# Performance work log

Measured on AMD Instinct MI355X. Metric: run time of the kernel, lower is better.

The kernel has to match this reference:

```python
import jax, jax.numpy as jnp
import numpy as np

B, N, C = 4, 4096, 768
H = 8
HD = C // H  # head_dim = 96
SCALE = HD ** -0.5
EPS = 1e-12  # torch F.normalize eps


def setup_inputs() -> dict:
    key = jax.random.key(0)
    ks = jax.random.split(key, 6)
    s = C ** -0.5
    return {
        "context_x": jax.random.normal(ks[0], (B, N, C), dtype=jnp.float32),
        "depth_x": jax.random.normal(ks[1], (B, N, C), dtype=jnp.float32),
        "Wq": jax.random.normal(ks[2], (C, C), dtype=jnp.float32) * s,
        "Wkv": jax.random.normal(ks[3], (C, 2 * C), dtype=jnp.float32) * s,
        "Wproj": jax.random.normal(ks[4], (C, C), dtype=jnp.float32) * s,
        "bproj": jax.random.normal(ks[5], (C,), dtype=jnp.float32) * 0.01,
    }


def _l2norm(x):
    # matches torch.nn.functional.normalize(x, dim=-1)
    n = jnp.sqrt(jnp.sum(x * x, axis=-1, keepdims=True))
    return x / jnp.maximum(n, EPS)


def reference(context_x, depth_x, Wq, Wkv, Wproj, bproj):
    b, n, c = context_x.shape
    # projections
    q = (context_x @ Wq).reshape(b, n, H, HD).transpose(0, 2, 3, 1)  # [B,H,hd,N]
    kv = (depth_x @ Wkv).reshape(b, n, 2, H, HD)
    k = kv[:, :, 0].transpose(0, 2, 3, 1)  # [B,H,hd,N]
    v = kv[:, :, 1].transpose(0, 2, 3, 1)  # [B,H,hd,N]
    # cosine-normalize over the token axis (last dim after transpose)
    q = _l2norm(q)
    k = _l2norm(k)
    # channel-attention (cross-covariance): attn is [B,H,hd,hd]
    attn = jnp.einsum("bhdn,bhen->bhde", q, k) * SCALE
    attn = jax.nn.softmax(attn, axis=-1)
    x = jnp.einsum("bhde,bhen->bhdn", attn, v)  # [B,H,hd,N]
    x = x.transpose(0, 3, 1, 2).reshape(b, n, c)  # [B,N,C]
    return x @ Wproj + bproj
```

## Files before the change

kernel.cpp:

```cpp
#include <hip/hip_runtime.h>


using bf16x8 = __attribute__((ext_vector_type(8))) short;
using f32x4  = __attribute__((ext_vector_type(4))) float;

#define SCALE_ 0.10206207261596575f

__device__ __forceinline__ unsigned short f2bf(float f) {
    unsigned int u = __builtin_bit_cast(unsigned int, f);
    u += 0x7FFFu + ((u >> 16) & 1u);
    return (unsigned short)(u >> 16);
}
__device__ __forceinline__ float bf2f(unsigned short h) {
    unsigned int u = ((unsigned int)h) << 16;
    return __builtin_bit_cast(float, u);
}

__device__ __forceinline__ void glds16(const unsigned short* g, unsigned short* l) {
    __builtin_amdgcn_global_load_lds(
        (const __attribute__((address_space(1))) void*)g,
        (__attribute__((address_space(3))) void*)l, 16, 0, 0);
}

__device__ __forceinline__ float ssq8(bf16x8 v) {
    uint4 u = __builtin_bit_cast(uint4, v);
    unsigned a[4] = {u.x, u.y, u.z, u.w};
    float s = 0.f;
    #pragma unroll
    for (int i = 0; i < 4; i++) {
        float lo = __builtin_bit_cast(float, a[i] << 16);
        float hi = __builtin_bit_cast(float, a[i] & 0xFFFF0000u);
        s += lo * lo + hi * hi;
    }
    return s;
}

__global__ void f32_to_bf16_k(const float* __restrict__ in,
                              unsigned short* __restrict__ out)
{
    size_t idx = ((size_t)blockIdx.x * 256 + threadIdx.x) * 8;
    float4 v0 = *(const float4*)&in[idx];
    float4 v1 = *(const float4*)&in[idx + 4];
    unsigned short h[8];
    h[0] = f2bf(v0.x); h[1] = f2bf(v0.y); h[2] = f2bf(v0.z); h[3] = f2bf(v0.w);
    h[4] = f2bf(v1.x); h[5] = f2bf(v1.y); h[6] = f2bf(v1.z); h[7] = f2bf(v1.w);
    *(bf16x8*)&out[idx] = *(bf16x8*)h;
}

__global__ void transpose_to_bf16(const float* __restrict__ W,
                                  unsigned short* __restrict__ Wt,
                                  int K, int N)
{
    __shared__ float tile[32][33];
    int n0 = blockIdx.x * 32, k0 = blockIdx.y * 32;
    int tx = threadIdx.x, ty = threadIdx.y;
    #pragma unroll
    for (int i = 0; i < 32; i += 8)
        tile[ty + i][tx] = W[(size_t)(k0 + ty + i) * N + n0 + tx];
    __syncthreads();
    #pragma unroll
    for (int i = 0; i < 32; i += 8)
        Wt[(size_t)(n0 + ty + i) * K + k0 + tx] = f2bf(tile[tx][ty + i]);
}


#define BAR __builtin_amdgcn_s_barrier()
#define VM(n) asm volatile("s_waitcnt vmcnt(" #n ")" ::: "memory")

#define ST_A(buf, tt, h) do { \
    _Pragma("unroll") \
    for (int c_ = 0; c_ < 2; c_++) \
        glds16(gA + (size_t)(((h) * 8 + w) * 16) * K + (size_t)(tt) * 64 + c_ * 32, \
               &As[buf][(c_ * 16 + (h) * 8 + w) * 512]); \
} while (0)

#define ST_B(buf, tt, h) do { \
    _Pragma("unroll") \
    for (int c_ = 0; c_ < 2; c_++) \
        glds16(gB + (size_t)(((h) * 8 + w) * 16) * K + (size_t)(tt) * 64 + c_ * 32, \
               &Bs[buf][(c_ * 16 + (h) * 8 + w) * 512]); \
} while (0)

#define RD_A(buf, mh) do { \
    _Pragma("unroll") \
    for (int i_ = 0; i_ < 4; i_++) \
    _Pragma("unroll") \
    for (int kk_ = 0; kk_ < 2; kk_++) \
        a[i_][kk_] = *(const bf16x8*)&As[buf][(kk_ * 16 + wr * 8 + (mh) * 4 + i_) * 512 + lane * 8]; \
} while (0)

#define RD_B(buf, nh) do { \
    _Pragma("unroll") \
    for (int j_ = 0; j_ < 2; j_++) \
    _Pragma("unroll") \
    for (int kk_ = 0; kk_ < 2; kk_++) \
        b[nh][j_][kk_] = *(const bf16x8*)&Bs[buf][(kk_ * 16 + wc * 4 + (nh) * 2 + j_) * 512 + lane * 8]; \
} while (0)

#define MM(mh, nh) do { \
    __builtin_amdgcn_s_setprio(1); \
    _Pragma("unroll") \
    for (int i_ = 0; i_ < 4; i_++) \
    _Pragma("unroll") \
    for (int j_ = 0; j_ < 2; j_++) \
    _Pragma("unroll") \
    for (int kk_ = 0; kk_ < 2; kk_++) \
        acc[(mh) * 4 + i_][(nh) * 2 + j_] = __builtin_amdgcn_mfma_f32_16x16x32_bf16( \
            a[i_][kk_], b[nh][j_][kk_], acc[(mh) * 4 + i_][(nh) * 2 + j_], 0, 0, 0); \
    __builtin_amdgcn_s_setprio(0); \
} while (0)

#define KITER(t0v, LAST) do { \
     RD_A(0, 0); RD_B(0, 0); ST_B(1, (t0v) + 1, 0); \
             BAR; MM(0, 0); BAR; \
     RD_B(0, 1); ST_B(1, (t0v) + 1, 1); \
             BAR; MM(0, 1); VM(6); BAR; \
     RD_A(0, 1); ST_A(1, (t0v) + 1, 1); \
             BAR; MM(1, 0); BAR; \
     if (!(LAST)) ST_A(0, (t0v) + 2, 0); \
             BAR; MM(1, 1); if (LAST) { VM(2); } else { VM(4); } BAR; \
     RD_A(1, 0); RD_B(1, 0); if (!(LAST)) ST_B(0, (t0v) + 2, 0); \
             BAR; MM(0, 0); BAR; \
     RD_B(1, 1); if (!(LAST)) ST_B(0, (t0v) + 2, 1); \
             BAR; MM(0, 1); if (LAST) { VM(0); } else { VM(6); } BAR; \
     RD_A(1, 1); if (!(LAST)) ST_A(0, (t0v) + 2, 1); \
             BAR; MM(1, 0); BAR; \
     if (!(LAST)) { ST_A(1, (t0v) + 3, 0); } \
             BAR; MM(1, 1); if (!(LAST)) { VM(4); } BAR; \
} while (0)

template<int MODE>
__global__ __launch_bounds__(512, 2) void gemm_bt(
    const unsigned short* __restrict__ A, const unsigned short* __restrict__ Bt,
    const float* __restrict__ bias, void* __restrict__ out0, void* __restrict__ out1,
    int M, int N, int K)
{
    __shared__ unsigned short As[2][32 * 512];
    __shared__ unsigned short Bs[2][32 * 512];

    const int Nt = gridDim.x, Mt = gridDim.y;
    const int lin = blockIdx.y * Nt + blockIdx.x;
    const int xcd = lin & 7, li = lin >> 3;
    const int band = Mt >> 3;
    const int mt = xcd * band + (li % band);
    const int nt = li / band;
    const int bm = mt * 256, bn = nt * 256;

    const int t = threadIdx.x, lane = t & 63, w = t >> 6;
    const int wr = w >> 2, wc = w & 3;
    const int mf = lane & 15, quad = lane >> 4;
    const int srow = lane & 15, skc = (lane >> 4) * 8;

    const unsigned short* gA = A  + (size_t)(bm + srow) * K + skc;
    const unsigned short* gB = Bt + (size_t)(bn + srow) * K + skc;

    f32x4 acc[8][4] = {};
    bf16x8 a[4][2], b[2][2][2];

    const int NIT = K >> 7;

    ST_A(0, 0, 0); ST_A(0, 0, 1); ST_B(0, 0, 0); ST_B(0, 0, 1); ST_A(1, 1, 0);
    VM(2); BAR;

    for (int it = 0; it < NIT - 1; ++it) { KITER(2 * it, false); }
    KITER(2 * (NIT - 1), true);

    if constexpr (MODE == 2) {
        float* C = (float*)out0;
        #pragma unroll
        for (int i = 0; i < 8; i++) {
            int row0 = bm + wr * 128 + i * 16 + quad * 4;
            #pragma unroll
            for (int j = 0; j < 4; j++) {
                int col = bn + wc * 64 + j * 16 + mf;
                float bv = bias[col];
                #pragma unroll
                for (int r = 0; r < 4; r++)
                    C[(size_t)(row0 + r) * N + col] = acc[i][j][r] + bv;
            }
        }
    } else {
        unsigned short* Tr = (unsigned short*)out0;
        unsigned short* Vb = (unsigned short*)out1;
        const bool kpart = (MODE == 0) || (bn < 768);
        #pragma unroll
        for (int i = 0; i < 8; i++) {
            int row0 = bm + wr * 128 + i * 16 + quad * 4;
            int bb = row0 >> 12, n = row0 & 4095;
            #pragma unroll
            for (int j = 0; j < 4; j++) {
                int c = bn + wc * 64 + j * 16 + mf;
                if (kpart) {
                    int h = (c * 683) >> 16;
                    int d = c - h * 96;
                    size_t o = ((size_t)((bb * 8 + h) * 96 + d)) * 4096 + n;
                    ushort4 v4;
                    v4.x = f2bf(acc[i][j][0]); v4.y = f2bf(acc[i][j][1]);
                    v4.z = f2bf(acc[i][j][2]); v4.w = f2bf(acc[i][j][3]);
                    *(ushort4*)&Tr[o] = v4;
                } else {
                    int cv = c - 768;
                    #pragma unroll
                    for (int r = 0; r < 4; r++)
                        Vb[(size_t)(row0 + r) * 768 + cv] = f2bf(acc[i][j][r]);
                }
            }
        }
    }
}

#undef KITER
#undef MM
#undef RD_A
#undef RD_B
#undef ST_A
#undef ST_B
#undef VM
#undef BAR

__global__ __launch_bounds__(256) void s_gemm(
    const unsigned short* __restrict__ Qt, const unsigned short* __restrict__ Kt,
    float* __restrict__ Spart, float* __restrict__ ssq)
{
    __shared__ unsigned short Qs[2][12 * 512];
    __shared__ unsigned short Ks[2][12 * 512];
    const int s = blockIdx.x, bh = blockIdx.y;
    const int t = threadIdx.x, lane = t & 63, w = t >> 6;
    const int m0 = (w >> 1) * 48, n0w = (w & 1) * 48;
    const int mf = lane & 15, quad = lane >> 4;
    const int srow = lane & 15, skc = (lane >> 4) * 8;
    const int nwin = s * 512;

    const unsigned short* Qg = Qt + (size_t)bh * 96 * 4096;
    const unsigned short* Kg = Kt + (size_t)bh * 96 * 4096;

    f32x4 acc[3][3] = {};
    float sq[3] = {0.f, 0.f, 0.f}, sk[3] = {0.f, 0.f, 0.f};

    #pragma unroll
    for (int c = 0; c < 3; c++) {
        int bi = w * 3 + c, kc = bi / 6, g = bi % 6;
        size_t go = (size_t)(g * 16 + srow) * 4096 + nwin + kc * 32 + skc;
        glds16(Qg + go, &Qs[0][bi * 512]);
        glds16(Kg + go, &Ks[0][bi * 512]);
    }

    for (int it = 0; it < 8; it++) {
        const int cur = it & 1;
        __syncthreads();
        if (it + 1 < 8) {
            const int nxt = cur ^ 1;
            const int nn = nwin + (it + 1) * 64;
            #pragma unroll
            for (int c = 0; c < 3; c++) {
                int bi = w * 3 + c, kc = bi / 6, g = bi % 6;
                size_t go = (size_t)(g * 16 + srow) * 4096 + nn + kc * 32 + skc;
                glds16(Qg + go, &Qs[nxt][bi * 512]);
                glds16(Kg + go, &Ks[nxt][bi * 512]);
            }
        }
        #pragma unroll
        for (int kk = 0; kk < 2; kk++) {
            bf16x8 a[3], b[3];
            #pragma unroll
            for (int i = 0; i < 3; i++)
                a[i] = *(const bf16x8*)&Qs[cur][(kk * 6 + (w >> 1) * 3 + i) * 512 + lane * 8];
            #pragma unroll
            for (int j = 0; j < 3; j++)
                b[j] = *(const bf16x8*)&Ks[cur][(kk * 6 + (w & 1) * 3 + j) * 512 + lane * 8];
            if ((w & 1) == 0) {
                #pragma unroll
                for (int i = 0; i < 3; i++) sq[i] += ssq8(a[i]);
            }
            if ((w >> 1) == 0) {
                #pragma unroll
                for (int j = 0; j < 3; j++) sk[j] += ssq8(b[j]);
            }
            #pragma unroll
            for (int i = 0; i < 3; i++)
                #pragma unroll
                for (int j = 0; j < 3; j++)
                    acc[i][j] = __builtin_amdgcn_mfma_f32_16x16x32_bf16(a[i], b[j], acc[i][j], 0, 0, 0);
        }
    }

    if ((w & 1) == 0) {
        #pragma unroll
        for (int i = 0; i < 3; i++) {
            float v = sq[i];
            v += __shfl_xor(v, 16, 64);
            v += __shfl_xor(v, 32, 64);
            if (lane < 16) atomicAdd(&ssq[bh * 96 + m0 + i * 16 + lane], v);
        }
    }
    if ((w >> 1) == 0) {
        #pragma unroll
        for (int j = 0; j < 3; j++) {
            float v = sk[j];
            v += __shfl_xor(v, 16, 64);
            v += __shfl_xor(v, 32, 64);
            if (lane < 16) atomicAdd(&ssq[3072 + bh * 96 + n0w + j * 16 + lane], v);
        }
    }

    float* outp = Spart + (size_t)(bh * 8 + s) * 9216;
    #pragma unroll
    for (int i = 0; i < 3; i++)
        #pragma unroll
        for (int j = 0; j < 3; j++) {
            int e  = n0w + j * 16 + mf;
            int d0 = m0 + i * 16 + quad * 4;
            #pragma unroll
            for (int r = 0; r < 4; r++)
                outp[(d0 + r) * 96 + e] = acc[i][j][r];
        }
}

__global__ __launch_bounds__(256) void softmax_k(
    const float* __restrict__ Spart, const float* __restrict__ ssq,
    unsigned short* __restrict__ P)
{
    const int bh = blockIdx.y;
    const int d  = blockIdx.x * 4 + (threadIdx.x >> 6);
    const int lane = threadIdx.x & 63;

    const float sr = SCALE_ / fmaxf(sqrtf(ssq[bh * 96 + d]), 1e-12f);

    const float* Sp = Spart + (size_t)bh * 8 * 9216 + d * 96;
    float sa = 0.f, sb = 0.f;
    #pragma unroll
    for (int ch = 0; ch < 8; ch++) {
        sa += Sp[ch * 9216 + lane];
        if (lane < 32) sb += Sp[ch * 9216 + 64 + lane];
    }
    float ka = 1.0f / fmaxf(sqrtf(ssq[3072 + bh * 96 + lane]), 1e-12f);
    float va = sa * sr * ka;
    float vb = -1e30f;
    if (lane < 32) {
        float kb = 1.0f / fmaxf(sqrtf(ssq[3072 + bh * 96 + 64 + lane]), 1e-12f);
        vb = sb * sr * kb;
    }

    float m = fmaxf(va, vb);
    #pragma unroll
    for (int off = 32; off >= 1; off >>= 1)
        m = fmaxf(m, __shfl_xor(m, off, 64));

    float ea = __expf(va - m);
    float eb = (lane < 32) ? __expf(vb - m) : 0.f;
    float ssum = ea + eb;
    #pragma unroll
    for (int off = 32; off >= 1; off >>= 1)
        ssum += __shfl_xor(ssum, off, 64);

    float inv = 1.0f / ssum;
    unsigned short* Pr = P + (size_t)bh * 9216 + d * 96;
    Pr[lane] = f2bf(ea * inv);
    if (lane < 32) Pr[64 + lane] = f2bf(eb * inv);
}

__global__ __launch_bounds__(256) void pv_gemm(
    const unsigned short* __restrict__ Vb, const unsigned short* __restrict__ P,
    unsigned short* __restrict__ X)
{
    __shared__ unsigned short Ps[96][104];
    int ntile = blockIdx.x, bh = blockIdx.y;
    int b = bh >> 3, h = bh & 7;
    int t = threadIdx.x, lane = t & 63, w = t >> 6;

    const unsigned short* Pg = P + (size_t)bh * 9216;
    #pragma unroll
    for (int i = 0; i < 9; i++) {
        int idx4 = t + 256 * i;
        int row = idx4 / 24, c4 = (idx4 - row * 24) * 4;
        *(ushort4*)&Ps[row][c4] = *(const ushort4*)&Pg[row * 96 + c4];
    }
    __syncthreads();

    const unsigned short* Vbase = Vb + (size_t)b * 4096 * 768 + h * 96;
    int mf = lane & 15, k8 = (lane >> 4) * 8;
    f32x4 acc[2][6] = {};
    #pragma unroll
    for (int k = 0; k < 3; k++) {
        bf16x8 a[2], bb[6];
        #pragma unroll
        for (int i = 0; i < 2; i++) {
            int row = ntile * 128 + w * 32 + i * 16 + mf;
            a[i] = *(const bf16x8*)&Vbase[(size_t)row * 768 + k * 32 + k8];
        }
        #pragma unroll
        for (int j = 0; j < 6; j++)
            bb[j] = *(const bf16x8*)&Ps[j * 16 + mf][k * 32 + k8];
        #pragma unroll
        for (int i = 0; i < 2; i++)
            #pragma unroll
            for (int j = 0; j < 6; j++)
                acc[i][j] = __builtin_amdgcn_mfma_f32_16x16x32_bf16(a[i], bb[j], acc[i][j], 0, 0, 0);
    }
    #pragma unroll
    for (int i = 0; i < 2; i++)
        #pragma unroll
        for (int j = 0; j < 6; j++)
            #pragma unroll
            for (int r = 0; r < 4; r++) {
                int n_tok = ntile * 128 + w * 32 + i * 16 + (lane >> 4) * 4 + r;
                int c = h * 96 + j * 16 + mf;
                X[((size_t)b * 4096 + n_tok) * 768 + c] = f2bf(acc[i][j][r]);
            }
}

extern "C" void kernel_launch(void* const* d_in, const int* in_sizes, int n_in,
                              void* d_out, int out_size, void* d_ws, size_t ws_size,
                              hipStream_t stream)
{
    (void)in_sizes; (void)n_in; (void)out_size; (void)ws_size;
    const float* ctx   = (const float*)d_in[0];
    const float* dep   = (const float*)d_in[1];
    const float* Wq    = (const float*)d_in[2];
    const float* Wkv   = (const float*)d_in[3];
    const float* Wproj = (const float*)d_in[4];
    const float* bproj = (const float*)d_in[5];
    float* out = (float*)d_out;

    char* p = (char*)d_ws;
    auto carve = [&](size_t bytes) {
        char* r = p;
        p += (bytes + 255) & ~(size_t)255;
        return r;
    };
    unsigned short* WqT    = (unsigned short*)carve((size_t)768 * 768 * 2);
    unsigned short* WkvT   = (unsigned short*)carve((size_t)1536 * 768 * 2);
    unsigned short* WprojT = (unsigned short*)carve((size_t)768 * 768 * 2);
    unsigned short* Qt     = (unsigned short*)carve((size_t)32 * 96 * 4096 * 2);
    unsigned short* Kt     = (unsigned short*)carve((size_t)32 * 96 * 4096 * 2);
    unsigned short* Vb     = (unsigned short*)carve((size_t)16384 * 768 * 2);
    unsigned short* Xb     = (unsigned short*)carve((size_t)16384 * 768 * 2);
    float*          ssq    = (float*)carve((size_t)2 * 3072 * 4);
    float*          Spart  = (float*)carve((size_t)32 * 8 * 9216 * 4);
    unsigned short* Pb     = (unsigned short*)carve((size_t)32 * 9216 * 2);
    unsigned short* depB   = (unsigned short*)carve((size_t)16384 * 768 * 2);
    unsigned short* ctxB   = Xb;

    hipMemsetAsync(ssq, 0, 2 * 3072 * 4, stream);

    f32_to_bf16_k<<<6144, 256, 0, stream>>>(ctx, ctxB);
    f32_to_bf16_k<<<6144, 256, 0, stream>>>(dep, depB);

    dim3 tb(32, 8);
    transpose_to_bf16<<<dim3(24, 24), tb, 0, stream>>>(Wq, WqT, 768, 768);
    transpose_to_bf16<<<dim3(48, 24), tb, 0, stream>>>(Wkv, WkvT, 768, 1536);
    transpose_to_bf16<<<dim3(24, 24), tb, 0, stream>>>(Wproj, WprojT, 768, 768);

    gemm_bt<0><<<dim3(3, 64), 512, 0, stream>>>(ctxB, WqT, nullptr, Qt, nullptr, 16384, 768, 768);
    gemm_bt<1><<<dim3(6, 64), 512, 0, stream>>>(depB, WkvT, nullptr, Kt, Vb, 16384, 1536, 768);

    s_gemm<<<dim3(8, 32), 256, 0, stream>>>(Qt, Kt, Spart, ssq);
    softmax_k<<<dim3(24, 32), 256, 0, stream>>>(Spart, ssq, Pb);
    pv_gemm<<<dim3(32, 32), 256, 0, stream>>>(Vb, Pb, Xb);
    gemm_bt<2><<<dim3(3, 64), 512, 0, stream>>>(Xb, WprojT, bproj, out, nullptr, 16384, 768, 768);
}
```

Measured before the change: 245.8 us.

## Shrink GEMM tiles to 256x128 and use triple-buffered LDS pipeline

The bf16 projection GEMM now uses a 256x128 output tile per block instead of 256x256, which doubles the grid size for better CU coverage on the 16384x768 GEMMs. The K-loop is restructured from a double-buffered, two-stage unrolled schedule into a three-stage LDS ring with K fixed at 768 (12 steps of 64). Each wave now holds a 64x64 accumulator, lowering register pressure. The cost is less operand reuse per tile, more B-tile reloads, and a hardcoded K.

```diff
diff --git a/kernel.cpp b/kernel.cpp
--- a/kernel.cpp
+++ b/kernel.cpp
@@ -5,6 +5,7 @@
 using f32x4  = __attribute__((ext_vector_type(4))) float;
 
 #define SCALE_ 0.10206207261596575f
+#define KD 768
 
 __device__ __forceinline__ unsigned short f2bf(float f) {
     unsigned int u = __builtin_bit_cast(unsigned int, f);
@@ -67,76 +68,56 @@
 #define BAR __builtin_amdgcn_s_barrier()
 #define VM(n) asm volatile("s_waitcnt vmcnt(" #n ")" ::: "memory")
 
-#define ST_A(buf, tt, h) do { \
+#define ST_A(sbase, tt, h) do { \
     _Pragma("unroll") \
     for (int c_ = 0; c_ < 2; c_++) \
-        glds16(gA + (size_t)(((h) * 8 + w) * 16) * K + (size_t)(tt) * 64 + c_ * 32, \
-               &As[buf][(c_ * 16 + (h) * 8 + w) * 512]); \
+        glds16(gA + (size_t)(((h) * 8 + w) * 16) * KD + (tt) * 64 + c_ * 32, \
+               (sbase) + (c_ * 16 + (h) * 8 + w) * 512); \
 } while (0)
 
-#define ST_B(buf, tt, h) do { \
+#define ST_B(sbase, tt) do { \
     _Pragma("unroll") \
     for (int c_ = 0; c_ < 2; c_++) \
-        glds16(gB + (size_t)(((h) * 8 + w) * 16) * K + (size_t)(tt) * 64 + c_ * 32, \
-               &Bs[buf][(c_ * 16 + (h) * 8 + w) * 512]); \
+        glds16(gB + (size_t)(w * 16) * KD + (tt) * 64 + c_ * 32, \
+               (sbase) + (c_ * 8 + w) * 512); \
 } while (0)
 
-#define RD_A(buf, mh) do { \
-    _Pragma("unroll") \
-    for (int i_ = 0; i_ < 4; i_++) \
+#define RD_A(cbase, mh) do { \
+    _Pragma("unroll") \
+    for (int i_ = 0; i_ < 2; i_++) \
     _Pragma("unroll") \
     for (int kk_ = 0; kk_ < 2; kk_++) \
-        a[i_][kk_] = *(const bf16x8*)&As[buf][(kk_ * 16 + wr * 8 + (mh) * 4 + i_) * 512 + lane * 8]; \
+        a[i_][kk_] = *(const bf16x8*)&(cbase)[(kk_ * 16 + wr * 4 + (mh) * 2 + i_) * 512 + lane * 8]; \
 } while (0)
 
-#define RD_B(buf, nh) do { \
+#define RD_B(cbase, nh) do { \
     _Pragma("unroll") \
     for (int j_ = 0; j_ < 2; j_++) \
     _Pragma("unroll") \
     for (int kk_ = 0; kk_ < 2; kk_++) \
-        b[nh][j_][kk_] = *(const bf16x8*)&Bs[buf][(kk_ * 16 + wc * 4 + (nh) * 2 + j_) * 512 + lane * 8]; \
+        b[nh][j_][kk_] = *(const bf16x8*)&(cbase)[(kk_ * 8 + wc * 4 + (nh) * 2 + j_) * 512 + lane * 8]; \
 } while (0)
 
 #define MM(mh, nh) do { \
     __builtin_amdgcn_s_setprio(1); \
     _Pragma("unroll") \
-    for (int i_ = 0; i_ < 4; i_++) \
+    for (int i_ = 0; i_ < 2; i_++) \
     _Pragma("unroll") \
     for (int j_ = 0; j_ < 2; j_++) \
     _Pragma("unroll") \
     for (int kk_ = 0; kk_ < 2; kk_++) \
-        acc[(mh) * 4 + i_][(nh) * 2 + j_] = __builtin_amdgcn_mfma_f32_16x16x32_bf16( \
-            a[i_][kk_], b[nh][j_][kk_], acc[(mh) * 4 + i_][(nh) * 2 + j_], 0, 0, 0); \
+        acc[(mh) * 2 + i_][(nh) * 2 + j_] = __builtin_amdgcn_mfma_f32_16x16x32_bf16( \
+            a[i_][kk_], b[nh][j_][kk_], acc[(mh) * 2 + i_][(nh) * 2 + j_], 0, 0, 0); \
     __builtin_amdgcn_s_setprio(0); \
-} while (0)
-
-#define KITER(t0v, LAST) do { \
-     RD_A(0, 0); RD_B(0, 0); ST_B(1, (t0v) + 1, 0); \
-             BAR; MM(0, 0); BAR; \
-     RD_B(0, 1); ST_B(1, (t0v) + 1, 1); \
-             BAR; MM(0, 1); VM(6); BAR; \
-     RD_A(0, 1); ST_A(1, (t0v) + 1, 1); \
-             BAR; MM(1, 0); BAR; \
-     if (!(LAST)) ST_A(0, (t0v) + 2, 0); \
-             BAR; MM(1, 1); if (LAST) { VM(2); } else { VM(4); } BAR; \
-     RD_A(1, 0); RD_B(1, 0); if (!(LAST)) ST_B(0, (t0v) + 2, 0); \
-             BAR; MM(0, 0); BAR; \
-     RD_B(1, 1); if (!(LAST)) ST_B(0, (t0v) + 2, 1); \
-             BAR; MM(0, 1); if (LAST) { VM(0); } else { VM(6); } BAR; \
-     RD_A(1, 1); if (!(LAST)) ST_A(0, (t0v) + 2, 1); \
-             BAR; MM(1, 0); BAR; \
-     if (!(LAST)) { ST_A(1, (t0v) + 3, 0); } \
-             BAR; MM(1, 1); if (!(LAST)) { VM(4); } BAR; \
 } while (0)
 
 template<int MODE>
 __global__ __launch_bounds__(512, 2) void gemm_bt(
     const unsigned short* __restrict__ A, const unsigned short* __restrict__ Bt,
     const float* __restrict__ bias, void* __restrict__ out0, void* __restrict__ out1,
-    int M, int N, int K)
-{
-    __shared__ unsigned short As[2][32 * 512];
-    __shared__ unsigned short Bs[2][32 * 512];
+    int M, int N)
+{
+    __shared__ unsigned short S[3 * 24576];
 
     const int Nt = gridDim.x, Mt = gridDim.y;
     const int lin = blockIdx.y * Nt + blockIdx.x;
@@ -144,32 +125,54 @@
     const int band = Mt >> 3;
     const int mt = xcd * band + (li % band);
     const int nt = li / band;
-    const int bm = mt * 256, bn = nt * 256;
+    const int bm = mt * 256, bn = nt * 128;
 
     const int t = threadIdx.x, lane = t & 63, w = t >> 6;
-    const int wr = w >> 2, wc = w & 3;
+    const int wr = w >> 1, wc = w & 1;
     const int mf = lane & 15, quad = lane >> 4;
-    const int srow = lane & 15, skc = (lane >> 4) * 8;
-
-    const unsigned short* gA = A  + (size_t)(bm + srow) * K + skc;
-    const unsigned short* gB = Bt + (size_t)(bn + srow) * K + skc;
-
-    f32x4 acc[8][4] = {};
-    bf16x8 a[4][2], b[2][2][2];
-
-    const int NIT = K >> 7;
-
-    ST_A(0, 0, 0); ST_A(0, 0, 1); ST_B(0, 0, 0); ST_B(0, 0, 1); ST_A(1, 1, 0);
-    VM(2); BAR;
-
-    for (int it = 0; it < NIT - 1; ++it) { KITER(2 * it, false); }
-    KITER(2 * (NIT - 1), true);
+
+    const unsigned short* gA = A  + (size_t)(bm + (lane & 15)) * KD + (lane >> 4) * 8;
+    const unsigned short* gB = Bt + (size_t)(bn + (lane & 15)) * KD + (lane >> 4) * 8;
+
+    f32x4 acc[4][4] = {};
+    bf16x8 a[2][2], b[2][2][2];
+
+    {
+        unsigned short* a0 = S;                  unsigned short* b0 = S + 16384;
+        unsigned short* a1 = S + 24576;          unsigned short* b1 = S + 24576 + 16384;
+        ST_A(a0, 0, 0); ST_A(a0, 0, 1); ST_B(b0, 0);
+        ST_A(a1, 1, 0); ST_A(a1, 1, 1); ST_B(b1, 1);
+    }
+    VM(6);
+    BAR;
+
+    unsigned cur = 0;
+    for (int tt = 0; tt < 12; ++tt) {
+        unsigned short* cA = S + cur * 24576;
+        unsigned short* cB = cA + 16384;
+        unsigned sg = cur + 2; if (sg >= 3) sg -= 3;
+        unsigned short* sA = S + sg * 24576;
+        unsigned short* sB = sA + 16384;
+        const bool st = (tt <= 9);
+
+        RD_A(cA, 0); RD_B(cB, 0); if (st) ST_A(sA, tt + 2, 0);
+        BAR; MM(0, 0); BAR;
+        RD_B(cB, 1); if (st) ST_A(sA, tt + 2, 1);
+        BAR; MM(0, 1); BAR;
+        RD_A(cA, 1); if (st) ST_B(sB, tt + 2);
+        BAR; MM(1, 0); BAR;
+        MM(1, 1);
+        if (tt < 10) { VM(6); }
+        else if (tt == 10) { VM(0); }
+        BAR;
+        cur = cur + 1; if (cur == 3) cur = 0;
+    }
 
     if constexpr (MODE == 2) {
         float* C = (float*)out0;
         #pragma unroll
-        for (int i = 0; i < 8; i++) {
-            int row0 = bm + wr * 128 + i * 16 + quad * 4;
+        for (int i = 0; i < 4; i++) {
+            int row0 = bm + wr * 64 + i * 16 + quad * 4;
             #pragma unroll
             for (int j = 0; j < 4; j++) {
                 int col = bn + wc * 64 + j * 16 + mf;
@@ -184,8 +187,8 @@
         unsigned short* Vb = (unsigned short*)out1;
         const bool kpart = (MODE == 0) || (bn < 768);
         #pragma unroll
-        for (int i = 0; i < 8; i++) {
-            int row0 = bm + wr * 128 + i * 16 + quad * 4;
+        for (int i = 0; i < 4; i++) {
+            int row0 = bm + wr * 64 + i * 16 + quad * 4;
             int bb = row0 >> 12, n = row0 & 4095;
             #pragma unroll
             for (int j = 0; j < 4; j++) {
@@ -209,7 +212,6 @@
     }
 }
 
-#undef KITER
 #undef MM
 #undef RD_A
 #undef RD_B
@@ -451,11 +453,11 @@
     transpose_to_bf16<<<dim3(48, 24), tb, 0, stream>>>(Wkv, WkvT, 768, 1536);
     transpose_to_bf16<<<dim3(24, 24), tb, 0, stream>>>(Wproj, WprojT, 768, 768);
 
-    gemm_bt<0><<<dim3(3, 64), 512, 0, stream>>>(ctxB, WqT, nullptr, Qt, nullptr, 16384, 768, 768);
-    gemm_bt<1><<<dim3(6, 64), 512, 0, stream>>>(depB, WkvT, nullptr, Kt, Vb, 16384, 1536, 768);
+    gemm_bt<0><<<dim3(6, 64), 512, 0, stream>>>(ctxB, WqT, nullptr, Qt, nullptr, 16384, 768);
+    gemm_bt<1><<<dim3(12, 64), 512, 0, stream>>>(depB, WkvT, nullptr, Kt, Vb, 16384, 1536);
 
     s_gemm<<<dim3(8, 32), 256, 0, stream>>>(Qt, Kt, Spart, ssq);
     softmax_k<<<dim3(24, 32), 256, 0, stream>>>(Spart, ssq, Pb);
     pv_gemm<<<dim3(32, 32), 256, 0, stream>>>(Vb, Pb, Xb);
-    gemm_bt<2><<<dim3(3, 64), 512, 0, stream>>>(Xb, WprojT, bproj, out, nullptr, 16384, 768, 768);
-}
+    gemm_bt<2><<<dim3(6, 64), 512, 0, stream>>>(Xb, WprojT, bproj, out, nullptr, 16384, 768);
+}
```

Result: faster. 226.9 us (-7.7%).

## Deepen GEMM prefetch pipeline and specialize K to compile-time constant

Applied to the files above, without the earlier changes.

Reworks the double-buffered GEMM schedule so that more global-to-LDS loads are in flight, prefetching both halves of the next A and B tiles earlier and relaxing vmcnt waits. The staging layout is remapped so each wave's load rows line up with the rows it later reads. K is hard-coded to 768, so address arithmetic and the loop trip count become constants. This gives up generality in K and depends on the reordered wait counts being correct for every stage.

```diff
diff --git a/kernel.cpp b/kernel.cpp
--- a/kernel.cpp
+++ b/kernel.cpp
@@ -5,6 +5,7 @@
 using f32x4  = __attribute__((ext_vector_type(4))) float;
 
 #define SCALE_ 0.10206207261596575f
+#define KD 768
 
 __device__ __forceinline__ unsigned short f2bf(float f) {
     unsigned int u = __builtin_bit_cast(unsigned int, f);
@@ -68,17 +69,19 @@
 #define VM(n) asm volatile("s_waitcnt vmcnt(" #n ")" ::: "memory")
 
 #define ST_A(buf, tt, h) do { \
+    const int r16a_ = (w >> 2) * 8 + (h) * 4 + (w & 3); \
     _Pragma("unroll") \
     for (int c_ = 0; c_ < 2; c_++) \
-        glds16(gA + (size_t)(((h) * 8 + w) * 16) * K + (size_t)(tt) * 64 + c_ * 32, \
-               &As[buf][(c_ * 16 + (h) * 8 + w) * 512]); \
+        glds16(gA + (size_t)(r16a_ * 16) * KD + (tt) * 64 + c_ * 32, \
+               &As[buf][(c_ * 16 + r16a_) * 512]); \
 } while (0)
 
 #define ST_B(buf, tt, h) do { \
+    const int r16b_ = (w >> 1) * 4 + (h) * 2 + (w & 1); \
     _Pragma("unroll") \
     for (int c_ = 0; c_ < 2; c_++) \
-        glds16(gB + (size_t)(((h) * 8 + w) * 16) * K + (size_t)(tt) * 64 + c_ * 32, \
-               &Bs[buf][(c_ * 16 + (h) * 8 + w) * 512]); \
+        glds16(gB + (size_t)(r16b_ * 16) * KD + (tt) * 64 + c_ * 32, \
+               &Bs[buf][(c_ * 16 + r16b_) * 512]); \
 } while (0)
 
 #define RD_A(buf, mh) do { \
@@ -111,29 +114,29 @@
 } while (0)
 
 #define KITER(t0v, LAST) do { \
-     RD_A(0, 0); RD_B(0, 0); ST_B(1, (t0v) + 1, 0); \
-             BAR; MM(0, 0); BAR; \
-     RD_B(0, 1); ST_B(1, (t0v) + 1, 1); \
-             BAR; MM(0, 1); VM(6); BAR; \
-     RD_A(0, 1); ST_A(1, (t0v) + 1, 1); \
+     RD_A(0, 0); RD_B(0, 0); ST_A(1, (t0v) + 1, 1); \
+             BAR; MM(0, 0); VM(10); BAR; \
+     RD_B(0, 1); if (!(LAST)) ST_A(0, (t0v) + 2, 0); \
+             BAR; MM(0, 1); if (LAST) { VM(8); } else { VM(10); } BAR; \
+     RD_A(0, 1); if (!(LAST)) ST_B(0, (t0v) + 2, 0); \
              BAR; MM(1, 0); BAR; \
-     if (!(LAST)) ST_A(0, (t0v) + 2, 0); \
-             BAR; MM(1, 1); if (LAST) { VM(2); } else { VM(4); } BAR; \
-     RD_A(1, 0); RD_B(1, 0); if (!(LAST)) ST_B(0, (t0v) + 2, 0); \
-             BAR; MM(0, 0); BAR; \
-     RD_B(1, 1); if (!(LAST)) ST_B(0, (t0v) + 2, 1); \
-             BAR; MM(0, 1); if (LAST) { VM(0); } else { VM(6); } BAR; \
-     RD_A(1, 1); if (!(LAST)) ST_A(0, (t0v) + 2, 1); \
+     if (!(LAST)) ST_B(0, (t0v) + 2, 1); \
+             BAR; MM(1, 1); if (LAST) { VM(4); } else { VM(10); } BAR; \
+     RD_A(1, 0); RD_B(1, 0); if (!(LAST)) ST_A(0, (t0v) + 2, 1); \
+             BAR; MM(0, 0); if (LAST) { VM(2); } else { VM(10); } BAR; \
+     RD_B(1, 1); if (!(LAST)) ST_A(1, (t0v) + 3, 0); \
+             BAR; MM(0, 1); if (LAST) { VM(0); } else { VM(10); } BAR; \
+     RD_A(1, 1); if (!(LAST)) ST_B(1, (t0v) + 3, 0); \
              BAR; MM(1, 0); BAR; \
-     if (!(LAST)) { ST_A(1, (t0v) + 3, 0); } \
-             BAR; MM(1, 1); if (!(LAST)) { VM(4); } BAR; \
+     if (!(LAST)) { ST_B(1, (t0v) + 3, 1); } \
+             BAR; MM(1, 1); if (!(LAST)) { VM(10); } BAR; \
 } while (0)
 
 template<int MODE>
 __global__ __launch_bounds__(512, 2) void gemm_bt(
     const unsigned short* __restrict__ A, const unsigned short* __restrict__ Bt,
     const float* __restrict__ bias, void* __restrict__ out0, void* __restrict__ out1,
-    int M, int N, int K)
+    int M, int N)
 {
     __shared__ unsigned short As[2][32 * 512];
     __shared__ unsigned short Bs[2][32 * 512];
@@ -149,21 +152,21 @@
     const int t = threadIdx.x, lane = t & 63, w = t >> 6;
     const int wr = w >> 2, wc = w & 3;
     const int mf = lane & 15, quad = lane >> 4;
-    const int srow = lane & 15, skc = (lane >> 4) * 8;
-
-    const unsigned short* gA = A  + (size_t)(bm + srow) * K + skc;
-    const unsigned short* gB = Bt + (size_t)(bn + srow) * K + skc;
+
+    const unsigned short* gA = A  + (size_t)(bm + (lane & 15)) * KD + (lane >> 4) * 8;
+    const unsigned short* gB = Bt + (size_t)(bn + (lane & 15)) * KD + (lane >> 4) * 8;
 
     f32x4 acc[8][4] = {};
     bf16x8 a[4][2], b[2][2][2];
 
-    const int NIT = K >> 7;
-
-    ST_A(0, 0, 0); ST_A(0, 0, 1); ST_B(0, 0, 0); ST_B(0, 0, 1); ST_A(1, 1, 0);
-    VM(2); BAR;
-
-    for (int it = 0; it < NIT - 1; ++it) { KITER(2 * it, false); }
-    KITER(2 * (NIT - 1), true);
+    ST_A(0, 0, 0); ST_B(0, 0, 0); ST_B(0, 0, 1); ST_A(0, 0, 1);
+    ST_A(1, 1, 0); ST_B(1, 1, 0); ST_B(1, 1, 1);
+    VM(10);
+    BAR;
+
+    #pragma unroll 1
+    for (int it = 0; it < 5; ++it) { KITER(2 * it, false); }
+    KITER(10, true);
 
     if constexpr (MODE == 2) {
         float* C = (float*)out0;
@@ -451,11 +454,11 @@
     transpose_to_bf16<<<dim3(48, 24), tb, 0, stream>>>(Wkv, WkvT, 768, 1536);
     transpose_to_bf16<<<dim3(24, 24), tb, 0, stream>>>(Wproj, WprojT, 768, 768);
 
-    gemm_bt<0><<<dim3(3, 64), 512, 0, stream>>>(ctxB, WqT, nullptr, Qt, nullptr, 16384, 768, 768);
-    gemm_bt<1><<<dim3(6, 64), 512, 0, stream>>>(depB, WkvT, nullptr, Kt, Vb, 16384, 1536, 768);
+    gemm_bt<0><<<dim3(3, 64), 512, 0, stream>>>(ctxB, WqT, nullptr, Qt, nullptr, 16384, 768);
+    gemm_bt<1><<<dim3(6, 64), 512, 0, stream>>>(depB, WkvT, nullptr, Kt, Vb, 16384, 1536);
 
     s_gemm<<<dim3(8, 32), 256, 0, stream>>>(Qt, Kt, Spart, ssq);
     softmax_k<<<dim3(24, 32), 256, 0, stream>>>(Spart, ssq, Pb);
     pv_gemm<<<dim3(32, 32), 256, 0, stream>>>(Vb, Pb, Xb);
-    gemm_bt<2><<<dim3(3, 64), 512, 0, stream>>>(Xb, WprojT, bproj, out, nullptr, 16384, 768, 768);
-}
+    gemm_bt<2><<<dim3(3, 64), 512, 0, stream>>>(Xb, WprojT, bproj, out, nullptr, 16384, 768);
+}
```

Measured after the change: 238.0 us. 1.03x faster.
